# Performance work log

Hardware: AMD Instinct MI355X
Metric: run time of the kernel (lower is better)

The kernel has to match this reference:

```python
import jax, jax.numpy as jnp
import numpy as np

N_IN = 100000
N_OUT = 100000
K = 27        # kernel_volume = 3^3 for 3D hypercube kernel
M = 50000     # matched (in,out) pairs per kernel offset
C_IN = 128
C_OUT = 128


def setup_inputs() -> dict:
    key = jax.random.key(0)
    k1, k2, k3, k4, k5 = jax.random.split(key, 5)
    features = jax.random.normal(k1, (N_IN, C_IN), dtype=jnp.float32)
    kernel = jax.random.normal(k2, (K, C_IN, C_OUT), dtype=jnp.float32) * (1.0 / np.sqrt(C_IN * K))
    bias = jax.random.normal(k3, (1, C_OUT), dtype=jnp.float32) * 0.01
    in_map = jax.random.randint(k4, (K, M), 0, N_IN, dtype=jnp.int32)
    out_map = jax.random.randint(k5, (K, M), 0, N_OUT, dtype=jnp.int32)
    return {"features": features, "kernel": kernel, "bias": bias,
            "in_map": in_map, "out_map": out_map, "n_out": N_OUT}


def reference(features, kernel, bias, in_map, out_map, n_out):
    # Sparse convolution: per-offset gather -> GEMM -> scatter-add.
    gathered = features[in_map]                          # [K, M, C_in]
    prod = jnp.einsum('kmc,kcd->kmd', gathered, kernel)  # [K, M, C_out]
    out = jnp.zeros((n_out, kernel.shape[-1]), dtype=features.dtype)
    out = out.at[out_map.reshape(-1)].add(prod.reshape(-1, kernel.shape[-1]))
    out = out + bias                                     # bias broadcast [1, C_out]
    return out
```

## Files before the change

kernel.cpp:

```cpp
#include <hip/hip_runtime.h>
#include <hip/hip_bf16.h>

typedef __attribute__((ext_vector_type(4))) float  f32x4;
typedef __attribute__((ext_vector_type(8))) short  bf16x8;
typedef __attribute__((ext_vector_type(4))) float  float4v;
typedef __attribute__((ext_vector_type(8))) unsigned short ushort8;
typedef __attribute__((ext_vector_type(2))) unsigned int uint2v;

#define CIO 128
#define BR  64
#define MAXTW 80
#define NB_MAX 4096
#define CSPLIT 8
#define NPASS 6
#define STAGE_CAP 14336

__device__ __forceinline__ unsigned short f2bf(float f) {
  unsigned int u = __float_as_uint(f);
  u = u + 0x7fffu + ((u >> 16) & 1u);
  return (unsigned short)(u >> 16);
}

__device__ __forceinline__ void wave_fence() {
  asm volatile("s_waitcnt lgkmcnt(0)" ::: "memory");
  __builtin_amdgcn_sched_barrier(0);
}

__global__ void prep_wswz(const float* __restrict__ W,
                          unsigned short* __restrict__ Wswz, int total) {
  int i = blockIdx.x * 256 + threadIdx.x;
  if (i >= total) return;
  int lane = i & 63;
  int nf   = (i >> 6) & 7;
  int kb   = (i >> 9) & 3;
  int k    = i >> 11;
  int n    = nf * 16 + (lane & 15);
  int c0   = kb * 32 + (lane >> 4) * 8;
  ushort8 v;
  #pragma unroll
  for (int e = 0; e < 8; ++e)
    v[e] = f2bf(W[k * 16384 + (c0 + e) * 128 + n]);
  *(ushort8*)(Wswz + (size_t)i * 8) = v;
}

__global__ void prep_fbf(const float* __restrict__ f,
                         unsigned short* __restrict__ fbf, int total8) {
  int i = blockIdx.x * 256 + threadIdx.x;
  if (i >= total8) return;
  const float4v* s = (const float4v*)(f + (size_t)i * 8);
  float4v v0 = s[0], v1 = s[1];
  ushort8 o;
  o[0] = f2bf(v0.x); o[1] = f2bf(v0.y); o[2] = f2bf(v0.z); o[3] = f2bf(v0.w);
  o[4] = f2bf(v1.x); o[5] = f2bf(v1.y); o[6] = f2bf(v1.z); o[7] = f2bf(v1.w);
  *(ushort8*)(fbf + (size_t)i * 8) = o;
}

__global__ __launch_bounds__(1024) void count27p(const int* __restrict__ out_map,
                                                 int* __restrict__ counts,
                                                 int M, int NB, int nkey) {
  __shared__ int h[NB_MAX];
  int k = blockIdx.x, s = blockIdx.y, t = threadIdx.x;
  for (int i = t; i < NB; i += 1024) h[i] = 0;
  __syncthreads();
  int m0 = (int)(((long)s * M) / CSPLIT), m1 = (int)(((long)(s + 1) * M) / CSPLIT);
  for (int m = m0 + t; m < m1; m += 1024)
    atomicAdd(&h[out_map[k * M + m] / BR], 1);
  __syncthreads();
  for (int i = t; i < NB; i += 1024)
    counts[s * nkey + k * NB + i] = h[i];
}

__global__ __launch_bounds__(1024) void scan_p1(const int* __restrict__ counts,
                                                int* __restrict__ offs,
                                                int* __restrict__ bsum, int nkey) {
  __shared__ int part[1024];
  const int t = threadIdx.x;
  const int i = blockIdx.x * 1024 + t;
  int v = 0;
  if (i < nkey) {
    #pragma unroll
    for (int sl = 0; sl < CSPLIT; ++sl) v += counts[sl * nkey + i];
  }
  part[t] = v;
  __syncthreads();
  for (int d = 1; d < 1024; d <<= 1) {
    int x = (t >= d) ? part[t - d] : 0;
    __syncthreads();
    part[t] += x;
    __syncthreads();
  }
  if (i < nkey) offs[i] = part[t] - v;
  if (t == 1023) bsum[blockIdx.x] = part[1023];
}
__global__ void scan_p2(int* __restrict__ bsum, int nb) {
  if (threadIdx.x == 0) {
    int run = 0;
    for (int i = 0; i < nb; ++i) { int c = bsum[i]; bsum[i] = run; run += c; }
    bsum[nb] = run;
  }
}
__global__ __launch_bounds__(1024) void scan_p3(int* __restrict__ offs,
                                                const int* __restrict__ bsum,
                                                int nkey, int nb) {
  const int i = blockIdx.x * 1024 + threadIdx.x;
  if (i < nkey) offs[i] += bsum[blockIdx.x];
  if (i == 0) offs[nkey] = bsum[nb];
}

__global__ __launch_bounds__(1024) void scatter27c(const int* __restrict__ in_map,
                                                   const int* __restrict__ out_map,
                                                   const int* __restrict__ offs,
                                                   unsigned int* __restrict__ sorted,
                                                   int M, int NB) {
  __shared__ unsigned int stage[STAGE_CAP];
  __shared__ int pos[700];
  const int k = blockIdx.x, p = blockIdx.y, t = threadIdx.x;
  const int b0 = (int)(((long)p * NB) / NPASS);
  const int b1 = (int)(((long)(p + 1) * NB) / NPASS);
  const int nb = b1 - b0;
  const int sbase = offs[k * NB + b0];
  const int send  = offs[k * NB + b1];
  const int size  = send - sbase;
  for (int i = t; i < nb; i += 1024) pos[i] = offs[k * NB + b0 + i] - sbase;
  __syncthreads();
  if (size <= STAGE_CAP) {
    for (int m = t; m < M; m += 1024) {
      int o = out_map[k * M + m];
      int bkt = o / BR;
      if (bkt >= b0 && bkt < b1) {
        int q = atomicAdd(&pos[bkt - b0], 1);
        stage[q] = ((unsigned int)in_map[k * M + m] << 7) | (unsigned int)(o & (BR - 1));
      }
    }
    __syncthreads();
    for (int i = t; i < size; i += 1024) sorted[sbase + i] = stage[i];
  } else {
    for (int m = t; m < M; m += 1024) {
      int o = out_map[k * M + m];
      int bkt = o / BR;
      if (bkt >= b0 && bkt < b1) {
        int q = atomicAdd(&pos[bkt - b0], 1);
        sorted[sbase + q] = ((unsigned int)in_map[k * M + m] << 7) | (unsigned int)(o & (BR - 1));
      }
    }
  }
}

__device__ __forceinline__ void load_w(const unsigned int* __restrict__ sorted,
                                       const int* tb, const int* te,
                                       int T, int ntiles, int l16,
                                       unsigned int& w0, unsigned int& w1) {
  w0 = 64u; w1 = 64u;
  if (T < ntiles) {
    int base = tb[T], e = te[T];
    int i0 = base + l16, i1 = base + 16 + l16;
    if (i0 < e) w0 = sorted[i0];
    if (i1 < e) w1 = sorted[i1];
  }
}
__device__ __forceinline__ void load_a(const unsigned short* __restrict__ fbf,
                                       unsigned int w0, unsigned int w1, int lk,
                                       bf16x8* a0, bf16x8* a1) {
  int in0 = (int)(w0 >> 7), in1 = (int)(w1 >> 7);
  #pragma unroll
  for (int kb = 0; kb < 4; ++kb) {
    a0[kb] = *(const bf16x8*)(fbf + (size_t)in0 * CIO + kb * 32 + lk * 8);
    a1[kb] = *(const bf16x8*)(fbf + (size_t)in1 * CIO + kb * 32 + lk * 8);
  }
}
__device__ __forceinline__ void compute_tile_w(const unsigned short* __restrict__ wk,
                                               const bf16x8 a0[4], const bf16x8 a1[4],
                                               unsigned char* sg,
                                               int lane, int l16, int lk, int swz) {
  #pragma unroll
  for (int h = 0; h < 2; ++h) {
    f32x4 acc[2][4] = {};
    #pragma unroll
    for (int kb = 0; kb < 4; ++kb) {
      const unsigned short* wkb = wk + kb * 4096 + h * 2048;
      #pragma unroll
      for (int nf = 0; nf < 4; ++nf) {
        bf16x8 bfr = *(const bf16x8*)(wkb + nf * 512 + lane * 8);
        acc[0][nf] = __builtin_amdgcn_mfma_f32_16x16x32_bf16(a0[kb], bfr, acc[0][nf], 0, 0, 0);
        acc[1][nf] = __builtin_amdgcn_mfma_f32_16x16x32_bf16(a1[kb], bfr, acc[1][nf], 0, 0, 0);
      }
    }
    #pragma unroll
    for (int rg = 0; rg < 2; ++rg)
      #pragma unroll
      for (int nf = 0; nf < 4; ++nf) {
        unsigned int lo = f2bf(acc[rg][nf][0]) | ((unsigned int)f2bf(acc[rg][nf][1]) << 16);
        unsigned int hi = f2bf(acc[rg][nf][2]) | ((unsigned int)f2bf(acc[rg][nf][3]) << 16);
        int c  = h * 64 + nf * 16 + l16;
        int eb = (rg * 16 + lk * 4) * 2;
        *(uint2v*)&sg[c * 128 + (eb ^ swz)] = (uint2v){lo, hi};
      }
  }
}
__device__ __forceinline__ void reduce_w(const unsigned char* __restrict__ lrow,
                                         const unsigned char* __restrict__ sg,
                                         f32x4 racc[4][8],
                                         int l16, int lk, int swz) {
  unsigned long long lr8 = *(const unsigned long long*)&lrow[lk * 8];
  int eb8[8];
  #pragma unroll
  for (int j = 0; j < 8; ++j) eb8[j] = (int)((lr8 >> (8 * j)) & 255ull);
  union { unsigned int u[4]; bf16x8 v; } su[4];
  #pragma unroll
  for (int mt = 0; mt < 4; ++mt) {
    const int target = mt * 16 + l16;
    #pragma unroll
    for (int p = 0; p < 4; ++p)
      su[mt].u[p] = (eb8[2 * p] == target ? 0x3F80u : 0u) |
                    (eb8[2 * p + 1] == target ? 0x3F800000u : 0u);
  }
  const int eoff = (lk * 16) ^ swz;
  #pragma unroll
  for (int nf = 0; nf < 8; ++nf) {
    bf16x8 bq = *(const bf16x8*)&sg[(nf * 16 + l16) * 128 + eoff];
    #pragma unroll
    for (int mt = 0; mt < 4; ++mt)
      racc[mt][nf] = __builtin_amdgcn_mfma_f32_16x16x32_bf16(su[mt].v, bq, racc[mt][nf], 0, 0, 0);
  }
}

__global__ __launch_bounds__(64) void spconv_wave(
    const unsigned short* __restrict__ fbf,
    const unsigned short* __restrict__ Wswz,
    const unsigned int* __restrict__ sorted,
    const int* __restrict__ offs,
    const float* __restrict__ bias,
    float* __restrict__ out,
    int NB, int n_out, int KVOL) {
  __shared__ __align__(16) unsigned char stag[16384];
  __shared__ __align__(8)  unsigned char lrowb[2][32];
  __shared__ int tb[MAXTW], te[MAXTW];
  __shared__ unsigned char tkk[MAXTW];

  const int lane = threadIdx.x & 63;
  const int l16  = lane & 15;
  const int lk   = lane >> 4;
  const int swz  = (l16 & 7) << 4;
  const int bucket = blockIdx.x;

  int vs = 0, vc = 0;
  if (lane < KVOL) {
    vs = offs[lane * NB + bucket];
    vc = offs[lane * NB + bucket + 1] - vs;
  }
  int ntr = 0;
  for (int k = 0; k < KVOL; ++k) {
    int s = __shfl(vs, k), c = __shfl(vc, k);
    if (lane == 0) {
      for (int t = 0; t < c; t += 32)
        if (ntr < MAXTW) { tkk[ntr] = (unsigned char)k; tb[ntr] = s + t; te[ntr] = s + c; ++ntr; }
    }
  }
  const int nt = __shfl(ntr, 0);
  wave_fence();

  f32x4 racc[4][8];
  #pragma unroll
  for (int mt = 0; mt < 4; ++mt)
    #pragma unroll
    for (int nf = 0; nf < 8; ++nf) racc[mt][nf] = (f32x4){0.f, 0.f, 0.f, 0.f};

  unsigned int wA0, wA1, wB0, wB1;
  bf16x8 aA0[4], aA1[4], aB0[4], aB1[4];
  load_w(sorted, tb, te, 0, nt, l16, wA0, wA1);
  if (lk == 0) {
    lrowb[0][l16]      = (unsigned char)(wA0 & 127u);
    lrowb[0][16 + l16] = (unsigned char)(wA1 & 127u);
  }
  load_a(fbf, wA0, wA1, lk, aA0, aA1);
  load_w(sorted, tb, te, 1, nt, l16, wB0, wB1);

  for (int bt = 0; bt < nt; bt += 2) {
    wave_fence();
    compute_tile_w(Wswz + (size_t)tkk[bt] * 16384, aA0, aA1, stag, lane, l16, lk, swz);
    load_a(fbf, wB0, wB1, lk, aB0, aB1);
    load_w(sorted, tb, te, bt + 2, nt, l16, wA0, wA1);
    if (lk == 0) {
      lrowb[1][l16]      = (unsigned char)(wB0 & 127u);
      lrowb[1][16 + l16] = (unsigned char)(wB1 & 127u);
    }
    wave_fence();
    reduce_w(&lrowb[0][0], stag, racc, l16, lk, swz);

    wave_fence();
    if (bt + 1 < nt)
      compute_tile_w(Wswz + (size_t)tkk[bt + 1] * 16384, aB0, aB1, stag, lane, l16, lk, swz);
    load_a(fbf, wA0, wA1, lk, aA0, aA1);
    load_w(sorted, tb, te, bt + 3, nt, l16, wB0, wB1);
    if (lk == 0) {
      lrowb[0][l16]      = (unsigned char)(wA0 & 127u);
      lrowb[0][16 + l16] = (unsigned char)(wA1 & 127u);
    }
    wave_fence();
    reduce_w(&lrowb[1][0], stag, racc, l16, lk, swz);
  }

  {
    float bi[8];
    #pragma unroll
    for (int nf = 0; nf < 8; ++nf) bi[nf] = bias[nf * 16 + l16];
    #pragma unroll
    for (int mt = 0; mt < 4; ++mt)
      #pragma unroll
      for (int r = 0; r < 4; ++r) {
        int orow = bucket * BR + mt * 16 + lk * 4 + r;
        if (orow < n_out) {
          #pragma unroll
          for (int nf = 0; nf < 8; ++nf)
            out[(size_t)orow * CIO + nf * 16 + l16] = racc[mt][nf][r] + bi[nf];
        }
      }
  }
}

__global__ void prep_weights(const float* __restrict__ W,
                             unsigned short* __restrict__ Wt, int total) {
  int idx = blockIdx.x * 256 + threadIdx.x;
  if (idx >= total) return;
  int k  = idx >> 14;
  int n  = (idx >> 7) & 127;
  int kk = idx & 127;
  Wt[idx] = f2bf(W[k * 16384 + kk * 128 + n]);
}
__global__ void init_bias(float* __restrict__ out,
                          const float* __restrict__ bias, int total4) {
  int idx = blockIdx.x * 256 + threadIdx.x;
  if (idx >= total4) return;
  float4v b = ((const float4v*)bias)[idx & 31];
  ((float4v*)out)[idx] = b;
}
__global__ __launch_bounds__(256) void spconv_mfma_legacy(
    const float* __restrict__ features, const unsigned short* __restrict__ Wt,
    const int* __restrict__ in_map, const int* __restrict__ out_map,
    float* __restrict__ out, int M) {
  const int ky = blockIdx.y, m0 = blockIdx.x * 64, tid = threadIdx.x;
  __shared__ unsigned short Alds[64 * CIO];
  __shared__ unsigned short Blds[CIO * CIO];
  {
    const ushort8* src = (const ushort8*)(Wt + ky * 16384);
    #pragma unroll
    for (int i = 0; i < 8; ++i) {
      int chunk = tid + i * 256, byte = chunk * 16;
      int row = byte >> 8, off = byte & 255, sw = off ^ ((row & 7) << 4);
      *(ushort8*)((char*)Blds + row * 256 + sw) = src[chunk];
    }
  }
  {
    int r = tid >> 2, q = tid & 3, m = m0 + r;
    unsigned short tmp[32];
    if (m < M) {
      int frow = in_map[ky * M + m];
      const float4v* src = (const float4v*)(features + frow * CIO + q * 32);
      #pragma unroll
      for (int i = 0; i < 8; ++i) {
        float4v v = src[i];
        tmp[i*4+0]=f2bf(v.x); tmp[i*4+1]=f2bf(v.y); tmp[i*4+2]=f2bf(v.z); tmp[i*4+3]=f2bf(v.w);
      }
    } else {
      #pragma unroll
      for (int i = 0; i < 32; ++i) tmp[i] = 0;
    }
    #pragma unroll
    for (int c = 0; c < 4; ++c) {
      int off = q * 64 + c * 16, sw = off ^ ((r & 7) << 4);
      *(ushort8*)((char*)Alds + r * 256 + sw) = *(ushort8*)(tmp + c * 8);
    }
  }
  __syncthreads();
  const int wid = tid >> 6, lane = tid & 63;
  const int wm = wid >> 1, wn = wid & 1, l16 = lane & 15, lk = lane >> 4;
  f32x4 acc[2][4] = {};
  #pragma unroll
  for (int kb = 0; kb < CIO; kb += 32) {
    bf16x8 af[2], bfr[4];
    #pragma unroll
    for (int mf = 0; mf < 2; ++mf) {
      int row = wm * 32 + mf * 16 + l16, off = (kb + lk * 8) * 2;
      int sw = off ^ ((row & 7) << 4);
      af[mf] = *(const bf16x8*)((const char*)Alds + row * 256 + sw);
    }
    #pragma unroll
    for (int nf = 0; nf < 4; ++nf) {
      int n = wn * 64 + nf * 16 + l16, off = (kb + lk * 8) * 2;
      int sw = off ^ ((n & 7) << 4);
      bfr[nf] = *(const bf16x8*)((const char*)Blds + n * 256 + sw);
    }
    #pragma unroll
    for (int mf = 0; mf < 2; ++mf)
      #pragma unroll
      for (int nf = 0; nf < 4; ++nf)
        acc[mf][nf] = __builtin_amdgcn_mfma_f32_16x16x32_bf16(af[mf], bfr[nf], acc[mf][nf], 0, 0, 0);
  }
  #pragma unroll
  for (int mf = 0; mf < 2; ++mf)
    #pragma unroll
    for (int r = 0; r < 4; ++r) {
      int mrow = wm * 32 + mf * 16 + lk * 4 + r, m = m0 + mrow;
      if (m < M) {
        int orow = out_map[ky * M + m];
        float* dst = out + orow * CIO + wn * 64 + l16;
        #pragma unroll
        for (int nf = 0; nf < 4; ++nf) unsafeAtomicAdd(dst + nf * 16, acc[mf][nf][r]);
      }
    }
}

static inline size_t align256(size_t x) { return (x + 255) & ~(size_t)255; }

extern "C" void kernel_launch(void* const* d_in, const int* in_sizes, int n_in,
                              void* d_out, int out_size, void* d_ws, size_t ws_size,
                              hipStream_t stream) {
  const float* features = (const float*)d_in[0];
  const float* W        = (const float*)d_in[1];
  const float* bias     = (const float*)d_in[2];
  const int*   in_map   = (const int*)d_in[3];
  const int*   out_map  = (const int*)d_in[4];
  float*       out      = (float*)d_out;

  const int KVOL  = in_sizes[1] / (CIO * CIO);
  const int M     = in_sizes[3] / KVOL;
  const int n_out = out_size / CIO;
  const int N_IN  = in_sizes[0] / CIO;
  const int NB    = (n_out + BR - 1) / BR;
  const int NKEY  = KVOL * NB;
  const size_t KM = (size_t)KVOL * M;

  const size_t s_wswz = (size_t)KVOL * CIO * CIO * 2;
  const size_t o_cnt  = align256(s_wswz);
  const size_t o_offs = align256(o_cnt + (size_t)CSPLIT * NKEY * 4);
  const size_t o_bsum = align256(o_offs + ((size_t)NKEY + 1) * 4);
  const size_t o_sort = align256(o_bsum + 4096 * 4);
  const size_t o_fbf  = align256(o_sort + KM * 4);
  const size_t need   = o_fbf + (size_t)N_IN * CIO * 2;

  if (NB <= NB_MAX && KVOL <= 32 && ws_size >= need) {
    unsigned short* Wswz   = (unsigned short*)d_ws;
    int*            cnt    = (int*)((char*)d_ws + o_cnt);
    int*            offs   = (int*)((char*)d_ws + o_offs);
    int*            bsum   = (int*)((char*)d_ws + o_bsum);
    unsigned int*   sorted = (unsigned int*)((char*)d_ws + o_sort);
    unsigned short* fbf    = (unsigned short*)((char*)d_ws + o_fbf);

    int wtot = KVOL * 4 * 8 * 64;
    prep_wswz<<<(wtot + 255) / 256, 256, 0, stream>>>(W, Wswz, wtot);
    int total8 = N_IN * CIO / 8;
    prep_fbf<<<(total8 + 255) / 256, 256, 0, stream>>>(features, fbf, total8);
    count27p<<<dim3(KVOL, CSPLIT), 1024, 0, stream>>>(out_map, cnt, M, NB, NKEY);

    const int nsb = (NKEY + 1023) / 1024;
    scan_p1<<<nsb, 1024, 0, stream>>>(cnt, offs, bsum, NKEY);
    scan_p2<<<1, 64, 0, stream>>>(bsum, nsb);
    scan_p3<<<nsb, 1024, 0, stream>>>(offs, bsum, NKEY, nsb);

    scatter27c<<<dim3(KVOL, NPASS), 1024, 0, stream>>>(in_map, out_map, offs, sorted, M, NB);

    spconv_wave<<<NB, 64, 0, stream>>>(fbf, Wswz, sorted, offs, bias, out,
                                       NB, n_out, KVOL);
  } else {
    unsigned short* Wt = (unsigned short*)d_ws;
    if (ws_size < s_wswz) return;
    int wtot = KVOL * CIO * CIO;
    prep_weights<<<(wtot + 255) / 256, 256, 0, stream>>>(W, Wt, wtot);
    int total4 = out_size / 4;
    init_bias<<<(total4 + 255) / 256, 256, 0, stream>>>(out, bias, total4);
    dim3 grid((M + 63) / 64, KVOL);
    spconv_mfma_legacy<<<grid, 256, 0, stream>>>(features, Wt, in_map, out_map, out, M);
  }
}
```

Baseline: 285.7 us.

## Split output channels across two waves per bucket to double grid parallelism

Each bucket is now handled by two single-wave blocks, each computing half of the 128 output channels. The grid doubles, per-wave accumulator registers and LDS staging halve, and occupancy should rise. In exchange, gathered feature rows, sorted indices and tile metadata are loaded twice, once by each half-block, which adds gather traffic.

Result: slower. 306.6 us (+7.3%).

```diff
diff --git a/kernel.cpp b/kernel.cpp
--- a/kernel.cpp
+++ b/kernel.cpp
@@ -168,38 +168,35 @@
     a1[kb] = *(const bf16x8*)(fbf + (size_t)in1 * CIO + kb * 32 + lk * 8);
   }
 }
-__device__ __forceinline__ void compute_tile_w(const unsigned short* __restrict__ wk,
+__device__ __forceinline__ void compute_tile_h(const unsigned short* __restrict__ wk,
                                                const bf16x8 a0[4], const bf16x8 a1[4],
-                                               unsigned char* sg,
+                                               unsigned char* sg, int half,
                                                int lane, int l16, int lk, int swz) {
-  #pragma unroll
-  for (int h = 0; h < 2; ++h) {
-    f32x4 acc[2][4] = {};
-    #pragma unroll
-    for (int kb = 0; kb < 4; ++kb) {
-      const unsigned short* wkb = wk + kb * 4096 + h * 2048;
-      #pragma unroll
-      for (int nf = 0; nf < 4; ++nf) {
-        bf16x8 bfr = *(const bf16x8*)(wkb + nf * 512 + lane * 8);
-        acc[0][nf] = __builtin_amdgcn_mfma_f32_16x16x32_bf16(a0[kb], bfr, acc[0][nf], 0, 0, 0);
-        acc[1][nf] = __builtin_amdgcn_mfma_f32_16x16x32_bf16(a1[kb], bfr, acc[1][nf], 0, 0, 0);
-      }
-    }
-    #pragma unroll
-    for (int rg = 0; rg < 2; ++rg)
-      #pragma unroll
-      for (int nf = 0; nf < 4; ++nf) {
-        unsigned int lo = f2bf(acc[rg][nf][0]) | ((unsigned int)f2bf(acc[rg][nf][1]) << 16);
-        unsigned int hi = f2bf(acc[rg][nf][2]) | ((unsigned int)f2bf(acc[rg][nf][3]) << 16);
-        int c  = h * 64 + nf * 16 + l16;
-        int eb = (rg * 16 + lk * 4) * 2;
-        *(uint2v*)&sg[c * 128 + (eb ^ swz)] = (uint2v){lo, hi};
-      }
-  }
-}
-__device__ __forceinline__ void reduce_w(const unsigned char* __restrict__ lrow,
+  f32x4 acc[2][4] = {};
+  #pragma unroll
+  for (int kb = 0; kb < 4; ++kb) {
+    const unsigned short* wkb = wk + kb * 4096 + half * 2048;
+    #pragma unroll
+    for (int nf = 0; nf < 4; ++nf) {
+      bf16x8 bfr = *(const bf16x8*)(wkb + nf * 512 + lane * 8);
+      acc[0][nf] = __builtin_amdgcn_mfma_f32_16x16x32_bf16(a0[kb], bfr, acc[0][nf], 0, 0, 0);
+      acc[1][nf] = __builtin_amdgcn_mfma_f32_16x16x32_bf16(a1[kb], bfr, acc[1][nf], 0, 0, 0);
+    }
+  }
+  #pragma unroll
+  for (int rg = 0; rg < 2; ++rg)
+    #pragma unroll
+    for (int nf = 0; nf < 4; ++nf) {
+      unsigned int lo = f2bf(acc[rg][nf][0]) | ((unsigned int)f2bf(acc[rg][nf][1]) << 16);
+      unsigned int hi = f2bf(acc[rg][nf][2]) | ((unsigned int)f2bf(acc[rg][nf][3]) << 16);
+      int c  = nf * 16 + l16;
+      int eb = (rg * 16 + lk * 4) * 2;
+      *(uint2v*)&sg[c * 128 + (eb ^ swz)] = (uint2v){lo, hi};
+    }
+}
+__device__ __forceinline__ void reduce_h(const unsigned char* __restrict__ lrow,
                                          const unsigned char* __restrict__ sg,
-                                         f32x4 racc[4][8],
+                                         f32x4 racc[4][4],
                                          int l16, int lk, int swz) {
   unsigned long long lr8 = *(const unsigned long long*)&lrow[lk * 8];
   int eb8[8];
@@ -216,7 +213,7 @@
   }
   const int eoff = (lk * 16) ^ swz;
   #pragma unroll
-  for (int nf = 0; nf < 8; ++nf) {
+  for (int nf = 0; nf < 4; ++nf) {
     bf16x8 bq = *(const bf16x8*)&sg[(nf * 16 + l16) * 128 + eoff];
     #pragma unroll
     for (int mt = 0; mt < 4; ++mt)
@@ -232,7 +229,7 @@
     const float* __restrict__ bias,
     float* __restrict__ out,
     int NB, int n_out, int KVOL) {
-  __shared__ __align__(16) unsigned char stag[16384];
+  __shared__ __align__(16) unsigned char stag[8192];
   __shared__ __align__(8)  unsigned char lrowb[2][32];
   __shared__ int tb[MAXTW], te[MAXTW];
   __shared__ unsigned char tkk[MAXTW];
@@ -241,7 +238,8 @@
   const int l16  = lane & 15;
   const int lk   = lane >> 4;
   const int swz  = (l16 & 7) << 4;
-  const int bucket = blockIdx.x;
+  const int bucket = blockIdx.x >> 1;
+  const int half   = blockIdx.x & 1;
 
   int vs = 0, vc = 0;
   if (lane < KVOL) {
@@ -259,11 +257,11 @@
   const int nt = __shfl(ntr, 0);
   wave_fence();
 
-  f32x4 racc[4][8];
+  f32x4 racc[4][4];
   #pragma unroll
   for (int mt = 0; mt < 4; ++mt)
     #pragma unroll
-    for (int nf = 0; nf < 8; ++nf) racc[mt][nf] = (f32x4){0.f, 0.f, 0.f, 0.f};
+    for (int nf = 0; nf < 4; ++nf) racc[mt][nf] = (f32x4){0.f, 0.f, 0.f, 0.f};
 
   unsigned int wA0, wA1, wB0, wB1;
   bf16x8 aA0[4], aA1[4], aB0[4], aB1[4];
@@ -277,7 +275,7 @@
 
   for (int bt = 0; bt < nt; bt += 2) {
     wave_fence();
-    compute_tile_w(Wswz + (size_t)tkk[bt] * 16384, aA0, aA1, stag, lane, l16, lk, swz);
+    compute_tile_h(Wswz + (size_t)tkk[bt] * 16384, aA0, aA1, stag, half, lane, l16, lk, swz);
     load_a(fbf, wB0, wB1, lk, aB0, aB1);
     load_w(sorted, tb, te, bt + 2, nt, l16, wA0, wA1);
     if (lk == 0) {
@@ -285,11 +283,11 @@
       lrowb[1][16 + l16] = (unsigned char)(wB1 & 127u);
     }
     wave_fence();
-    reduce_w(&lrowb[0][0], stag, racc, l16, lk, swz);
+    reduce_h(&lrowb[0][0], stag, racc, l16, lk, swz);
 
     wave_fence();
     if (bt + 1 < nt)
-      compute_tile_w(Wswz + (size_t)tkk[bt + 1] * 16384, aB0, aB1, stag, lane, l16, lk, swz);
+      compute_tile_h(Wswz + (size_t)tkk[bt + 1] * 16384, aB0, aB1, stag, half, lane, l16, lk, swz);
     load_a(fbf, wA0, wA1, lk, aA0, aA1);
     load_w(sorted, tb, te, bt + 3, nt, l16, wB0, wB1);
     if (lk == 0) {
@@ -297,13 +295,13 @@
       lrowb[0][16 + l16] = (unsigned char)(wA1 & 127u);
     }
     wave_fence();
-    reduce_w(&lrowb[1][0], stag, racc, l16, lk, swz);
+    reduce_h(&lrowb[1][0], stag, racc, l16, lk, swz);
   }
 
   {
-    float bi[8];
-    #pragma unroll
-    for (int nf = 0; nf < 8; ++nf) bi[nf] = bias[nf * 16 + l16];
+    float bi[4];
+    #pragma unroll
+    for (int nf = 0; nf < 4; ++nf) bi[nf] = bias[half * 64 + nf * 16 + l16];
     #pragma unroll
     for (int mt = 0; mt < 4; ++mt)
       #pragma unroll
@@ -311,8 +309,8 @@
         int orow = bucket * BR + mt * 16 + lk * 4 + r;
         if (orow < n_out) {
           #pragma unroll
-          for (int nf = 0; nf < 8; ++nf)
-            out[(size_t)orow * CIO + nf * 16 + l16] = racc[mt][nf][r] + bi[nf];
+          for (int nf = 0; nf < 4; ++nf)
+            out[(size_t)orow * CIO + half * 64 + nf * 16 + l16] = racc[mt][nf][r] + bi[nf];
         }
       }
   }
@@ -459,8 +457,8 @@
 
     scatter27c<<<dim3(KVOL, NPASS), 1024, 0, stream>>>(in_map, out_map, offs, sorted, M, NB);
 
-    spconv_wave<<<NB, 64, 0, stream>>>(fbf, Wswz, sorted, offs, bias, out,
-                                       NB, n_out, KVOL);
+    spconv_wave<<<NB * 2, 64, 0, stream>>>(fbf, Wswz, sorted, offs, bias, out,
+                                           NB, n_out, KVOL);
   } else {
     unsigned short* Wt = (unsigned short*)d_ws;
     if (ws_size < s_wswz) return;
```

## Double-buffer staging LDS and overlap reduce reads with next tile compute

Applied to the files above, without the earlier changes.

Splits the reduce step into an LDS-read issue phase and an MFMA phase, and double-buffers the staging LDS tile so the next tile's compute can write one buffer while the reduce reads the other. The wave_fence barriers between compute and reduce are removed, so LDS reads, global loads and MFMAs can interleave. LDS use doubles to about 32KB per block, which may lower occupancy, and register pressure rises from holding eight bf16x8 values across the compute. Without the explicit fences, correctness depends on the implicit LDS ordering within a single wave.

Measured after the change: 378.7 us. 1.33x slower.

```diff
diff --git a/kernel.cpp b/kernel.cpp
--- a/kernel.cpp
+++ b/kernel.cpp
@@ -197,15 +197,26 @@
       }
   }
 }
-__device__ __forceinline__ void reduce_w(const unsigned char* __restrict__ lrow,
-                                         const unsigned char* __restrict__ sg,
-                                         f32x4 racc[4][8],
-                                         int l16, int lk, int swz) {
-  unsigned long long lr8 = *(const unsigned long long*)&lrow[lk * 8];
+
+struct RVals { unsigned long long lr8; bf16x8 b[8]; };
+
+__device__ __forceinline__ RVals reduce_issue(const unsigned char* __restrict__ lrow,
+                                              const unsigned char* __restrict__ sg,
+                                              int l16, int lk, int swz) {
+  RVals v;
+  v.lr8 = *(const unsigned long long*)&lrow[lk * 8];
+  const int eoff = (lk * 16) ^ swz;
+  #pragma unroll
+  for (int nf = 0; nf < 8; ++nf)
+    v.b[nf] = *(const bf16x8*)&sg[(nf * 16 + l16) * 128 + eoff];
+  return v;
+}
+__device__ __forceinline__ void reduce_fma(const RVals& v, f32x4 racc[4][8],
+                                           int l16) {
   int eb8[8];
   #pragma unroll
-  for (int j = 0; j < 8; ++j) eb8[j] = (int)((lr8 >> (8 * j)) & 255ull);
-  union { unsigned int u[4]; bf16x8 v; } su[4];
+  for (int j = 0; j < 8; ++j) eb8[j] = (int)((v.lr8 >> (8 * j)) & 255ull);
+  union { unsigned int u[4]; bf16x8 s; } su[4];
   #pragma unroll
   for (int mt = 0; mt < 4; ++mt) {
     const int target = mt * 16 + l16;
@@ -214,14 +225,11 @@
       su[mt].u[p] = (eb8[2 * p] == target ? 0x3F80u : 0u) |
                     (eb8[2 * p + 1] == target ? 0x3F800000u : 0u);
   }
-  const int eoff = (lk * 16) ^ swz;
-  #pragma unroll
-  for (int nf = 0; nf < 8; ++nf) {
-    bf16x8 bq = *(const bf16x8*)&sg[(nf * 16 + l16) * 128 + eoff];
+  #pragma unroll
+  for (int nf = 0; nf < 8; ++nf)
     #pragma unroll
     for (int mt = 0; mt < 4; ++mt)
-      racc[mt][nf] = __builtin_amdgcn_mfma_f32_16x16x32_bf16(su[mt].v, bq, racc[mt][nf], 0, 0, 0);
-  }
+      racc[mt][nf] = __builtin_amdgcn_mfma_f32_16x16x32_bf16(su[mt].s, v.b[nf], racc[mt][nf], 0, 0, 0);
 }
 
 __global__ __launch_bounds__(64) void spconv_wave(
@@ -232,7 +240,7 @@
     const float* __restrict__ bias,
     float* __restrict__ out,
     int NB, int n_out, int KVOL) {
-  __shared__ __align__(16) unsigned char stag[16384];
+  __shared__ __align__(16) unsigned char stag[2][16384];
   __shared__ __align__(8)  unsigned char lrowb[2][32];
   __shared__ int tb[MAXTW], te[MAXTW];
   __shared__ unsigned char tkk[MAXTW];
@@ -265,39 +273,48 @@
     #pragma unroll
     for (int nf = 0; nf < 8; ++nf) racc[mt][nf] = (f32x4){0.f, 0.f, 0.f, 0.f};
 
-  unsigned int wA0, wA1, wB0, wB1;
-  bf16x8 aA0[4], aA1[4], aB0[4], aB1[4];
-  load_w(sorted, tb, te, 0, nt, l16, wA0, wA1);
-  if (lk == 0) {
-    lrowb[0][l16]      = (unsigned char)(wA0 & 127u);
-    lrowb[0][16 + l16] = (unsigned char)(wA1 & 127u);
-  }
-  load_a(fbf, wA0, wA1, lk, aA0, aA1);
-  load_w(sorted, tb, te, 1, nt, l16, wB0, wB1);
-
-  for (int bt = 0; bt < nt; bt += 2) {
-    wave_fence();
-    compute_tile_w(Wswz + (size_t)tkk[bt] * 16384, aA0, aA1, stag, lane, l16, lk, swz);
-    load_a(fbf, wB0, wB1, lk, aB0, aB1);
-    load_w(sorted, tb, te, bt + 2, nt, l16, wA0, wA1);
-    if (lk == 0) {
-      lrowb[1][l16]      = (unsigned char)(wB0 & 127u);
-      lrowb[1][16 + l16] = (unsigned char)(wB1 & 127u);
-    }
-    wave_fence();
-    reduce_w(&lrowb[0][0], stag, racc, l16, lk, swz);
-
-    wave_fence();
-    if (bt + 1 < nt)
-      compute_tile_w(Wswz + (size_t)tkk[bt + 1] * 16384, aB0, aB1, stag, lane, l16, lk, swz);
-    load_a(fbf, wA0, wA1, lk, aA0, aA1);
-    load_w(sorted, tb, te, bt + 3, nt, l16, wB0, wB1);
+  if (nt > 0) {
+    unsigned int wA0, wA1, wB0, wB1;
+    bf16x8 aA0[4], aA1[4], aB0[4], aB1[4];
+    load_w(sorted, tb, te, 0, nt, l16, wA0, wA1);
     if (lk == 0) {
       lrowb[0][l16]      = (unsigned char)(wA0 & 127u);
       lrowb[0][16 + l16] = (unsigned char)(wA1 & 127u);
     }
-    wave_fence();
-    reduce_w(&lrowb[1][0], stag, racc, l16, lk, swz);
+    load_a(fbf, wA0, wA1, lk, aA0, aA1);
+    load_w(sorted, tb, te, 1, nt, l16, wB0, wB1);
+    compute_tile_w(Wswz + (size_t)tkk[0] * 16384, aA0, aA1, stag[0], lane, l16, lk, swz);
+    load_a(fbf, wB0, wB1, lk, aB0, aB1);
+    load_w(sorted, tb, te, 2, nt, l16, wA0, wA1);
+
+    for (int bt = 0; bt < nt; bt += 2) {
+      {
+        RVals v = reduce_issue(&lrowb[0][0], stag[0], l16, lk, swz);
+        if (bt + 1 < nt)
+          compute_tile_w(Wswz + (size_t)tkk[bt + 1] * 16384, aB0, aB1, stag[1],
+                         lane, l16, lk, swz);
+        if (lk == 0) {
+          lrowb[1][l16]      = (unsigned char)(wB0 & 127u);
+          lrowb[1][16 + l16] = (unsigned char)(wB1 & 127u);
+        }
+        load_a(fbf, wA0, wA1, lk, aA0, aA1);
+        load_w(sorted, tb, te, bt + 3, nt, l16, wB0, wB1);
+        reduce_fma(v, racc, l16);
+      }
+      {
+        RVals v = reduce_issue(&lrowb[1][0], stag[1], l16, lk, swz);
+        if (bt + 2 < nt)
+          compute_tile_w(Wswz + (size_t)tkk[bt + 2] * 16384, aA0, aA1, stag[0],
+                         lane, l16, lk, swz);
+        if (lk == 0) {
+          lrowb[0][l16]      = (unsigned char)(wA0 & 127u);
+          lrowb[0][16 + l16] = (unsigned char)(wA1 & 127u);
+        }
+        load_a(fbf, wB0, wB1, lk, aB0, aB1);
+        load_w(sorted, tb, te, bt + 4, nt, l16, wA0, wA1);
+        reduce_fma(v, racc, l16);
+      }
+    }
   }
 
   {
```
